# Kernel tuning notes

Hardware: AMD Instinct MI355X
Metric: run time of the kernel (lower is better)

Reference implementation:

```python
import jax, jax.numpy as jnp
import numpy as np

KH, KW = 3, 3
STRIDE = 1
OUT_CH, IN_CH = 128, 64


def setup_inputs() -> dict:
    key = jax.random.key(0)
    k1, k2 = jax.random.split(key)
    x = jax.random.normal(k1, (32, 64, 64, 64), dtype=jnp.float32)
    # xavier_normal_ init: std = sqrt(2 / (fan_in + fan_out))
    fan_in = IN_CH * KH * KW
    fan_out = OUT_CH * KH * KW
    std = (2.0 / (fan_in + fan_out)) ** 0.5
    weight = jax.random.normal(k2, (OUT_CH, IN_CH, KH, KW), dtype=jnp.float32) * std
    bias = jnp.zeros((OUT_CH,), dtype=jnp.float32)
    return {"x": x, "weight": weight, "bias": bias}


def _extract_patches(x, kh, kw, stride):
    # Equivalent of F.unfold, laid out as [B, C, kh, kw, Oh, Ow]
    B, C, H, W = x.shape
    oh = (H - kh) // stride + 1
    ow = (W - kw) // stride + 1
    rows = []
    for i in range(kh):  # small fixed kernel loop
        cols = []
        for j in range(kw):
            cols.append(x[:, :, i:i + stride * oh:stride, j:j + stride * ow:stride])
        rows.append(jnp.stack(cols, axis=2))
    return jnp.stack(rows, axis=2)  # [B, C, kh, kw, Oh, Ow]


def reference(x, weight, bias):
    # --- weight normalization over (in_ch, kh, kw), guard zero norms ---
    nrm = jnp.sqrt(jnp.sum(weight * weight, axis=(1, 2, 3), keepdims=True))
    nrm = jnp.where(nrm == 0, jnp.ones_like(nrm), nrm)
    w = weight / nrm

    # --- conv2d forward (act = Identity) ---
    y = jax.lax.conv_general_dilated(
        x, w, window_strides=(STRIDE, STRIDE), padding='VALID',
        dimension_numbers=('NCHW', 'OIHW', 'NCHW'))
    y = y + bias[None, :, None, None]  # [B, K, Oh, Ow]

    # --- WTA Hebbian update (computed in no_grad in the original) ---
    patches = _extract_patches(x, KH, KW, STRIDE)  # [B, C, kh, kw, Oh, Ow]
    winners = jnp.argmax(y, axis=1)                # [B, Oh, Ow] winner channel per location
    mask = jax.nn.one_hot(winners, y.shape[1], dtype=y.dtype)  # [B, Oh, Ow, K]
    hebb = jnp.einsum('bhwk,bcijhw->kcij', mask, patches)       # masked outer-product reduction
    B = x.shape[0]
    L = y.shape[2] * y.shape[3]
    weight_update = hebb / (jnp.float32(B * L) + 1e-8)  # wta_mask.sum() == B*L
    return y, weight_update
```

## Files before the change

### kernel.cpp

```cpp
#include <hip/hip_runtime.h>
#include <math.h>

typedef __attribute__((ext_vector_type(8))) short bf16x8;
typedef __attribute__((ext_vector_type(4))) float f32x4;

#define IC 64
#define OC 128
#define OHW 62
#define LOCS (OHW*OHW)
#define BATCH 32
#define Y_SIZE (BATCH*OC*LOCS)
#define UPD_SIZE (OC*IC*9)

#define SWZ(w) (((w) & 7) << 3)

__device__ __forceinline__ unsigned short f2bf(float f) {
    unsigned u = __float_as_uint(f);
    unsigned r = (u + 0x7FFFu + ((u >> 16) & 1u)) >> 16;
    return (unsigned short)r;
}
__device__ __forceinline__ float bf2f(unsigned short h) {
    return __uint_as_float(((unsigned)h) << 16);
}
__device__ __forceinline__ unsigned packhi(unsigned u1, unsigned u0) {
    return __builtin_amdgcn_perm(u1, u0, 0x07060302u);
}

__global__ void wnorm_kernel(const float* __restrict__ w, short* __restrict__ wH) {
    int k = blockIdx.x;
    int c = threadIdx.x;
    const float* wp = w + ((size_t)k*IC + c)*9;
    float v[9]; float s = 0.f;
#pragma unroll
    for (int t = 0; t < 9; ++t) { v[t] = wp[t]; s += v[t]*v[t]; }
#pragma unroll
    for (int off = 32; off > 0; off >>= 1) s += __shfl_xor(s, off);
    float nrm = sqrtf(s);
    if (nrm == 0.f) nrm = 1.f;
    float inv = 1.f / nrm;
    const int ch = c >> 5, lg = (c >> 3) & 3, pos = c & 7;
#pragma unroll
    for (int t = 0; t < 9; ++t) {
        size_t off = ((size_t)((t*2 + ch)*4 + lg)*128 + k)*8 + pos;
        wH[off] = (short)f2bf(v[t]*inv);
    }
}

__global__ __launch_bounds__(256, 6) void conv_kernel(
    const float* __restrict__ x, const short* __restrict__ wH,
    const float* __restrict__ bias, float* __restrict__ y,
    int* __restrict__ winners)
{
    __shared__ short xh[3*66*64];
    __shared__ float biasL[OC];

    const int l = blockIdx.x;
    const int v = (l & 7)*248 + (l >> 3);
    const int b = v / OHW;
    const int oh = v - b*OHW;
    const int tid = threadIdx.x;
    if (tid < OC) biasL[tid] = bias[tid];

    float4 A0[6], A1[6];
#pragma unroll
    for (int q = 0; q < 6; ++q) {
        int it = tid + q*256;
        int wq = it & 15, c2 = (it >> 4) & 31, i = it >> 9;
        const float* p = x + (((size_t)(b*IC + c2*2))*64 + (oh + i))*64 + wq*4;
        A0[q] = *(const float4*)p;
        A1[q] = *(const float4*)(p + 4096);
    }
#pragma unroll
    for (int q = 0; q < 6; ++q) {
        int it = tid + q*256;
        int wq = it & 15, c2 = (it >> 4) & 31, i = it >> 9;
        int c = c2*2, w0 = wq*4;
        float f0[4] = {A0[q].x, A0[q].y, A0[q].z, A0[q].w};
        float f1[4] = {A1[q].x, A1[q].y, A1[q].z, A1[q].w};
#pragma unroll
        for (int jj = 0; jj < 4; ++jj) {
            int w = w0 + jj;
            unsigned u0 = __float_as_uint(f0[jj]);
            unsigned u1 = __float_as_uint(f1[jj]);
            unsigned r0 = u0 + 0x7FFFu + ((u0 >> 16) & 1u);
            unsigned r1 = u1 + 0x7FFFu + ((u1 >> 16) & 1u);
            unsigned hi = packhi(r1, r0);
            int e = (i*66 + w)*64 + c;
            int widx = (e ^ SWZ(w)) >> 1;
            ((unsigned*)xh)[widx] = hi;
        }
    }
    __syncthreads();

    const int lane = tid & 63, wv = tid >> 6;
    const int l15 = lane & 15, lg = lane >> 4;
    const int kbase = wv*32;

    f32x4 acc[2][4];
#pragma unroll
    for (int kf = 0; kf < 2; ++kf)
#pragma unroll
        for (int nf = 0; nf < 4; ++nf)
            acc[kf][nf] = (f32x4){0.f,0.f,0.f,0.f};

    bf16x8 pah[3][2];
#pragma unroll
    for (int ps = 0; ps < 2; ++ps)
#pragma unroll
        for (int kf = 0; kf < 2; ++kf) {
            int k = kbase + kf*16 + l15;
            pah[ps][kf] = *(const bf16x8*)(wH + ((size_t)(ps*4 + lg)*128 + k)*8);
        }

    __builtin_amdgcn_s_setprio(1);
#pragma unroll
    for (int s = 0; s < 18; ++s) {
        const int ij = s >> 1, ch = s & 1;
        const int i = ij / 3, j = ij % 3;
        const int cur = s % 3;
        if (s + 2 < 18) {
            const int nxt = (s + 2) % 3;
#pragma unroll
            for (int kf = 0; kf < 2; ++kf) {
                int k = kbase + kf*16 + l15;
                pah[nxt][kf] = *(const bf16x8*)(wH + ((size_t)((s+2)*4 + lg)*128 + k)*8);
            }
        }
#pragma unroll
        for (int nf = 0; nf < 4; ++nf) {
            int w = nf*16 + l15 + j;
            int e = (i*66 + w)*64 + ch*32 + lg*8;
            int si = e ^ SWZ(w);
            bf16x8 bh = *(const bf16x8*)(xh + si);
#pragma unroll
            for (int kf = 0; kf < 2; ++kf)
                acc[kf][nf] = __builtin_amdgcn_mfma_f32_16x16x32_bf16(pah[cur][kf], bh, acc[kf][nf], 0, 0, 0);
        }
    }
    __builtin_amdgcn_s_setprio(0);

    __syncthreads();
    float* redv = (float*)xh;
    int*   redi = ((int*)xh) + 256;

#pragma unroll
    for (int nf = 0; nf < 4; ++nf) {
        int n = nf*16 + l15;
        float vm = -3.4e38f; int im = 0;
#pragma unroll
        for (int kf = 0; kf < 2; ++kf)
#pragma unroll
            for (int r = 0; r < 4; ++r) {
                int k = kbase + kf*16 + lg*4 + r;
                float v2 = acc[kf][nf][r] + biasL[k];
                if (n < OHW) y[(((size_t)b*OC + k)*OHW + oh)*OHW + n] = v2;
                if (v2 > vm) { vm = v2; im = k; }
            }
        {
            float ov = __shfl_xor(vm, 16); int oi = __shfl_xor(im, 16);
            if (ov > vm || (ov == vm && oi < im)) { vm = ov; im = oi; }
            ov = __shfl_xor(vm, 32); oi = __shfl_xor(im, 32);
            if (ov > vm || (ov == vm && oi < im)) { vm = ov; im = oi; }
        }
        if (lg == 0) { redv[wv*64 + n] = vm; redi[wv*64 + n] = im; }
    }
    __syncthreads();
    if (tid < OHW) {
        float bv = redv[tid]; int bi = redi[tid];
#pragma unroll
        for (int wvv = 1; wvv < 4; ++wvv) {
            float v2 = redv[wvv*64 + tid]; int i2 = redi[wvv*64 + tid];
            if (v2 > bv || (v2 == bv && i2 < bi)) { bv = v2; bi = i2; }
        }
        winners[(size_t)b*LOCS + oh*OHW + tid] = bi;
    }
}

__global__ __launch_bounds__(512, 4) void hebb_kernel(
    const float* __restrict__ x, const int* __restrict__ winners,
    unsigned short* __restrict__ part, int G)
{
    __shared__ short xR[16*10*72];
    __shared__ int winL[8*64];

    const int bid = blockIdx.x;
    const int q = bid & 3, g = bid >> 2;
    const int tid = threadIdx.x;
    const int lane = tid & 63, wv = tid >> 6;
    const int l15 = lane & 15, lg = lane >> 4;
    const int myk = wv*16 + l15;

    int off0[3];
#pragma unroll
    for (int nf = 0; nf < 3; ++nf) {
        int npL = nf*16 + l15;
        int cL = npL / 3, i = npL % 3;
        off0[nf] = (cL*10 + i)*72;
    }

    f32x4 acc[3][3];
#pragma unroll
    for (int j = 0; j < 3; ++j)
#pragma unroll
        for (int nf = 0; nf < 3; ++nf)
            acc[j][nf] = (f32x4){0.f,0.f,0.f,0.f};

    for (int t = g; t < 256; t += G) {
        const int b = t >> 3, sub = t & 7;
        const int oh0 = sub*8;
        const int NR = (sub == 7) ? 6 : 8;
        const int rows = NR + 2;

        __syncthreads();
        for (int it = tid; it < 16*rows*16; it += 512) {
            int wq2 = it & 15;
            int t2 = it >> 4;
            int r = t2 % rows, cL = t2 / rows;
            const float* p = x + (((size_t)(b*IC + q*16 + cL))*64 + (oh0 + r))*64 + wq2*4;
            float4 a = *(const float4*)p;
            unsigned u0 = packhi(__float_as_uint(a.y), __float_as_uint(a.x));
            unsigned u1 = packhi(__float_as_uint(a.w), __float_as_uint(a.z));
            int e = (cL*10 + r)*72 + wq2*4;
            ((unsigned*)xR)[e >> 1]       = u0;
            ((unsigned*)xR)[(e >> 1) + 1] = u1;
        }
        for (int tt = tid; tt < NR*64; tt += 512) {
            int r = tt >> 6, ow = tt & 63;
            winL[tt] = (ow < OHW) ? winners[(size_t)b*LOCS + (oh0 + r)*OHW + ow] : -1;
        }
        __syncthreads();

        for (int r = 0; r < NR; ++r) {
#pragma unroll
            for (int h = 0; h < 2; ++h) {
                const int base = h*32 + lg*8;
                const int* wrow = &winL[r*64];
                int wreg[8];
                *(int4*)&wreg[0] = *(const int4*)&wrow[base];
                *(int4*)&wreg[4] = *(const int4*)&wrow[base + 4];
                const int wm1 = (base >= 1) ? wrow[base-1] : -1;
                const int wm2 = (base >= 2) ? wrow[base-2] : -1;
                union U8 { unsigned u[4]; bf16x8 v; };
                bf16x8 am[3];
#pragma unroll
                for (int j = 0; j < 3; ++j) {
                    U8 tmp;
#pragma unroll
                    for (int p2 = 0; p2 < 4; ++p2) {
                        int t0 = p2*2, t1 = t0 + 1;
                        int s0 = (t0 >= j) ? wreg[t0-j] : ((j - t0 == 1) ? wm1 : wm2);
                        int s1 = (t1 >= j) ? wreg[t1-j] : ((j - t1 == 1) ? wm1 : wm2);
                        tmp.u[p2] = ((s0 == myk) ? 0x3F80u : 0u)
                                  | (((s1 == myk) ? 0x3F80u : 0u) << 16);
                    }
                    am[j] = tmp.v;
                }
#pragma unroll
                for (int nf = 0; nf < 3; ++nf) {
                    const bf16x8 bb = *(const bf16x8*)&xR[off0[nf] + r*72 + base];
#pragma unroll
                    for (int j = 0; j < 3; ++j)
                        acc[j][nf] = __builtin_amdgcn_mfma_f32_16x16x32_bf16(am[j], bb, acc[j][nf], 0, 0, 0);
                }
            }
        }
    }

    unsigned short* dst = part + (size_t)bid*(144*128);
#pragma unroll
    for (int j = 0; j < 3; ++j)
#pragma unroll
        for (int nf = 0; nf < 3; ++nf) {
            int npL = nf*16 + l15;
            int rowL = npL*3 + j;
            int kc   = wv*16 + lg*4;
            ushort4 o;
            o.x = f2bf(acc[j][nf][0]); o.y = f2bf(acc[j][nf][1]);
            o.z = f2bf(acc[j][nf][2]); o.w = f2bf(acc[j][nf][3]);
            *(ushort4*)(dst + rowL*128 + kc) = o;
        }
}

__global__ __launch_bounds__(256) void final1_kernel(const unsigned short* __restrict__ part,
                                                     float* __restrict__ tmp, int G, int NS) {
    int bid = blockIdx.x;
    int ob = bid % 288, ns = bid / 288;
    int t = ob*256 + threadIdx.x;
    int k = t & 127, row = t >> 7;
    int q = row / 144;
    int rowL = row - q*144;
    int g0 = ns*16, g1 = g0 + 16; if (g1 > G) g1 = G;
    float s = 0.f;
    for (int g = g0; g < g1; ++g)
        s += bf2f(part[((size_t)(g*4 + q))*(144*128) + rowL*128 + k]);
    tmp[(size_t)ns*UPD_SIZE + t] = s;
}

__global__ __launch_bounds__(256) void final2_kernel(const float* __restrict__ tmp,
                                                     float* __restrict__ upd, int NS) {
    int t = blockIdx.x*256 + threadIdx.x;
    int k = t & 127, row = t >> 7;
    float s = 0.f;
    for (int ns = 0; ns < NS; ++ns)
        s += tmp[(size_t)ns*UPD_SIZE + t];
    upd[(size_t)k*576 + row] = s * (1.0f/123008.0f);
}

extern "C" void kernel_launch(void* const* d_in, const int* in_sizes, int n_in,
                              void* d_out, int out_size, void* d_ws, size_t ws_size,
                              hipStream_t stream) {
    const float* x    = (const float*)d_in[0];
    const float* w    = (const float*)d_in[1];
    const float* bias = (const float*)d_in[2];
    float* out = (float*)d_out;
    float* y   = out;
    float* upd = out + Y_SIZE;

    const size_t fixed = 147456 + 492032;
    short* wHs     = (short*)d_ws;
    int*   winners = (int*)((char*)d_ws + 147456);

    size_t avail = (ws_size > fixed) ? (ws_size - fixed) : 0;
    int G = 256;
    while (G > 1) {
        size_t need = (size_t)4*G*36864 + (size_t)((G + 15)/16)*294912;
        if (need <= avail) break;
        G >>= 1;
    }
    int NS = (G + 15)/16;

    unsigned short* part = (unsigned short*)((char*)d_ws + fixed);
    float* tmp = (float*)((char*)d_ws + fixed + (size_t)4*G*36864);

    wnorm_kernel<<<OC, IC, 0, stream>>>(w, wHs);
    conv_kernel<<<OHW*BATCH, 256, 0, stream>>>(x, wHs, bias, y, winners);
    hebb_kernel<<<4*G, 512, 0, stream>>>(x, winners, part, G);
    final1_kernel<<<288*NS, 256, 0, stream>>>(part, tmp, G, NS);
    final2_kernel<<<288, 256, 0, stream>>>(tmp, upd, NS);
}
```

Baseline: 95.66 us.

## Retile conv waves to 64x32 and batch hebb global loads before LDS stores

The conv kernel's four waves now each cover 64 output channels by 32 columns instead of 32 channels by all 64 columns. This halves the repeated LDS reads of the x tile per wave at the cost of twice the weight-fragment registers, so the occupancy hint drops from 6 to 4. The final argmax reduction now combines two wave partials instead of four. The hebb kernel issues all of its x and winner global loads into registers before converting and storing to LDS, giving more memory-level parallelism, and a reduction loop in final1 gets an unroll hint.

```diff
diff --git a/kernel.cpp b/kernel.cpp
--- a/kernel.cpp
+++ b/kernel.cpp
@@ -46,7 +46,7 @@
     }
 }
 
-__global__ __launch_bounds__(256, 6) void conv_kernel(
+__global__ __launch_bounds__(256, 4) void conv_kernel(
     const float* __restrict__ x, const short* __restrict__ wH,
     const float* __restrict__ bias, float* __restrict__ y,
     int* __restrict__ winners)
@@ -94,20 +94,21 @@
 
     const int lane = tid & 63, wv = tid >> 6;
     const int l15 = lane & 15, lg = lane >> 4;
-    const int kbase = wv*32;
-
-    f32x4 acc[2][4];
-#pragma unroll
-    for (int kf = 0; kf < 2; ++kf)
-#pragma unroll
-        for (int nf = 0; nf < 4; ++nf)
+    const int khalf = wv & 1, nhalf = wv >> 1;
+    const int kbase = khalf*64, nbase = nhalf*32;
+
+    f32x4 acc[4][2];
+#pragma unroll
+    for (int kf = 0; kf < 4; ++kf)
+#pragma unroll
+        for (int nf = 0; nf < 2; ++nf)
             acc[kf][nf] = (f32x4){0.f,0.f,0.f,0.f};
 
-    bf16x8 pah[3][2];
+    bf16x8 pah[3][4];
 #pragma unroll
     for (int ps = 0; ps < 2; ++ps)
 #pragma unroll
-        for (int kf = 0; kf < 2; ++kf) {
+        for (int kf = 0; kf < 4; ++kf) {
             int k = kbase + kf*16 + l15;
             pah[ps][kf] = *(const bf16x8*)(wH + ((size_t)(ps*4 + lg)*128 + k)*8);
         }
@@ -121,19 +122,19 @@
         if (s + 2 < 18) {
             const int nxt = (s + 2) % 3;
 #pragma unroll
-            for (int kf = 0; kf < 2; ++kf) {
+            for (int kf = 0; kf < 4; ++kf) {
                 int k = kbase + kf*16 + l15;
                 pah[nxt][kf] = *(const bf16x8*)(wH + ((size_t)((s+2)*4 + lg)*128 + k)*8);
             }
         }
 #pragma unroll
-        for (int nf = 0; nf < 4; ++nf) {
-            int w = nf*16 + l15 + j;
+        for (int nf = 0; nf < 2; ++nf) {
+            int w = nbase + nf*16 + l15 + j;
             int e = (i*66 + w)*64 + ch*32 + lg*8;
             int si = e ^ SWZ(w);
             bf16x8 bh = *(const bf16x8*)(xh + si);
 #pragma unroll
-            for (int kf = 0; kf < 2; ++kf)
+            for (int kf = 0; kf < 4; ++kf)
                 acc[kf][nf] = __builtin_amdgcn_mfma_f32_16x16x32_bf16(pah[cur][kf], bh, acc[kf][nf], 0, 0, 0);
         }
     }
@@ -144,11 +145,11 @@
     int*   redi = ((int*)xh) + 256;
 
 #pragma unroll
-    for (int nf = 0; nf < 4; ++nf) {
-        int n = nf*16 + l15;
+    for (int nf = 0; nf < 2; ++nf) {
+        int n = nbase + nf*16 + l15;
         float vm = -3.4e38f; int im = 0;
 #pragma unroll
-        for (int kf = 0; kf < 2; ++kf)
+        for (int kf = 0; kf < 4; ++kf)
 #pragma unroll
             for (int r = 0; r < 4; ++r) {
                 int k = kbase + kf*16 + lg*4 + r;
@@ -166,12 +167,10 @@
     }
     __syncthreads();
     if (tid < OHW) {
-        float bv = redv[tid]; int bi = redi[tid];
-#pragma unroll
-        for (int wvv = 1; wvv < 4; ++wvv) {
-            float v2 = redv[wvv*64 + tid]; int i2 = redi[wvv*64 + tid];
-            if (v2 > bv || (v2 == bv && i2 < bi)) { bv = v2; bi = i2; }
-        }
+        int w0 = (tid >> 5)*2;
+        float bv = redv[w0*64 + tid]; int bi = redi[w0*64 + tid];
+        float v2 = redv[(w0+1)*64 + tid]; int i2 = redi[(w0+1)*64 + tid];
+        if (v2 > bv || (v2 == bv && i2 < bi)) { bv = v2; bi = i2; }
         winners[(size_t)b*LOCS + oh*OHW + tid] = bi;
     }
 }
@@ -210,24 +209,42 @@
         const int oh0 = sub*8;
         const int NR = (sub == 7) ? 6 : 8;
         const int rows = NR + 2;
+        const int cnt = rows >> 1;
 
         __syncthreads();
-        for (int it = tid; it < 16*rows*16; it += 512) {
-            int wq2 = it & 15;
-            int t2 = it >> 4;
-            int r = t2 % rows, cL = t2 / rows;
-            const float* p = x + (((size_t)(b*IC + q*16 + cL))*64 + (oh0 + r))*64 + wq2*4;
-            float4 a = *(const float4*)p;
-            unsigned u0 = packhi(__float_as_uint(a.y), __float_as_uint(a.x));
-            unsigned u1 = packhi(__float_as_uint(a.w), __float_as_uint(a.z));
-            int e = (cL*10 + r)*72 + wq2*4;
-            ((unsigned*)xR)[e >> 1]       = u0;
-            ((unsigned*)xR)[(e >> 1) + 1] = u1;
-        }
-        for (int tt = tid; tt < NR*64; tt += 512) {
-            int r = tt >> 6, ow = tt & 63;
-            winL[tt] = (ow < OHW) ? winners[(size_t)b*LOCS + (oh0 + r)*OHW + ow] : -1;
-        }
+        float4 A[5];
+#pragma unroll
+        for (int q2 = 0; q2 < 5; ++q2) {
+            if (q2 < cnt) {
+                int it = tid + q2*512;
+                int wq2 = it & 15;
+                int t2 = it >> 4;
+                int r = t2 % rows, cL = t2 / rows;
+                const float* p = x + (((size_t)(b*IC + q*16 + cL))*64 + (oh0 + r))*64 + wq2*4;
+                A[q2] = *(const float4*)p;
+            }
+        }
+        int wval = -1;
+        const int haveW = tid < NR*64;
+        if (haveW) {
+            int r = tid >> 6, ow = tid & 63;
+            wval = (ow < OHW) ? winners[(size_t)b*LOCS + (oh0 + r)*OHW + ow] : -1;
+        }
+#pragma unroll
+        for (int q2 = 0; q2 < 5; ++q2) {
+            if (q2 < cnt) {
+                int it = tid + q2*512;
+                int wq2 = it & 15;
+                int t2 = it >> 4;
+                int r = t2 % rows, cL = t2 / rows;
+                unsigned u0 = packhi(__float_as_uint(A[q2].y), __float_as_uint(A[q2].x));
+                unsigned u1 = packhi(__float_as_uint(A[q2].w), __float_as_uint(A[q2].z));
+                int e = (cL*10 + r)*72 + wq2*4;
+                ((unsigned*)xR)[e >> 1]       = u0;
+                ((unsigned*)xR)[(e >> 1) + 1] = u1;
+            }
+        }
+        if (haveW) winL[tid] = wval;
         __syncthreads();
 
         for (int r = 0; r < NR; ++r) {
@@ -291,6 +308,7 @@
     int rowL = row - q*144;
     int g0 = ns*16, g1 = g0 + 16; if (g1 > G) g1 = G;
     float s = 0.f;
+#pragma unroll 4
     for (int g = g0; g < g1; ++g)
         s += bf2f(part[((size_t)(g*4 + q))*(144*128) + rowL*128 + k]);
     tmp[(size_t)ns*UPD_SIZE + t] = s;
```

New measurement: 90.20 us. 5.7% less time.
